# Optimization experiments

Hardware: AMD Instinct MI355X
Metric: run time of the kernel (lower is better)

## Reference

```python
import jax, jax.numpy as jnp
import numpy as np

N, TX, TZ, DX, DZ, DATT, DOUT = 8, 2048, 2048, 1024, 1024, 1024, 1024


def setup_inputs() -> dict:
    key = jax.random.key(0)
    ks = jax.random.split(key, 8)
    s = 0.02
    x = jax.random.normal(ks[0], (N, TX, DX), dtype=jnp.float32)
    z = jax.random.normal(ks[1], (N, TZ, DZ), dtype=jnp.float32)
    Wq = jax.random.normal(ks[2], (DX, DATT), dtype=jnp.float32) * s
    bq = jnp.zeros((DATT,), dtype=jnp.float32)
    Wk = jax.random.normal(ks[3], (DZ, DATT), dtype=jnp.float32) * s
    bk = jnp.zeros((DATT,), dtype=jnp.float32)
    Wv = jax.random.normal(ks[4], (DZ, DOUT), dtype=jnp.float32) * s
    bv = jnp.zeros((DOUT,), dtype=jnp.float32)
    # fixed boolean mask [Tx, Tz]; causal lower-triangular so no row is fully masked
    mask = jnp.tril(jnp.ones((TX, TZ), dtype=bool))
    return {"x": x, "z": z, "Wq": Wq, "bq": bq, "Wk": Wk, "bk": bk,
            "Wv": Wv, "bv": bv, "mask": mask}


def reference(x, z, Wq, bq, Wk, bk, Wv, bv, mask):
    Datt = Wq.shape[1]
    Q = x @ Wq + bq                      # [N, Tx, Datt]
    K = z @ Wk + bk                      # [N, Tz, Datt]
    V = z @ Wv + bv                      # [N, Tz, Dout]
    S = jnp.einsum('bxd,bzd->bxz', Q, K)  # [N, Tx, Tz]
    S = jnp.where(mask[None, :, :], S, -jnp.inf)
    A = jax.nn.softmax(S / jnp.sqrt(jnp.float32(Datt)), axis=-1)
    y = jnp.einsum('bxz,bzo->bxo', A, V)  # [N, Tx, Dout]
    return y
```

## Files before the change

### kernel.cpp

```cpp
#include <hip/hip_runtime.h>

typedef _Float16 f16;
typedef _Float16 f16x8 __attribute__((ext_vector_type(8)));
typedef _Float16 f16x4 __attribute__((ext_vector_type(4)));
typedef float    f32x4 __attribute__((ext_vector_type(4)));

constexpr int NB   = 8;
constexpr int T    = 2048;
constexpr int D    = 1024;
constexpr int NTRI = 136;

__device__ __forceinline__ void load_lds16(const f16* g, f16* l) {
    __builtin_amdgcn_global_load_lds(
        (const __attribute__((address_space(1))) void*)g,
        (__attribute__((address_space(3))) void*)l, 16, 0, 0);
}

__global__ __launch_bounds__(256) void cast_transpose_w(
    const float* __restrict__ W0, const float* __restrict__ W1,
    const float* __restrict__ W2, f16* __restrict__ Wt)
{
    __shared__ f16 tile[32][33];
    const int which = blockIdx.z;
    const float* W = which == 0 ? W0 : (which == 1 ? W1 : W2);
    f16* dst = Wt + (size_t)which * D * D;
    const int c0 = blockIdx.x * 32, r0 = blockIdx.y * 32;
    const int tx = threadIdx.x & 31, ty = threadIdx.x >> 5;
    #pragma unroll
    for (int i = 0; i < 32; i += 8)
        tile[ty + i][tx] = (f16)W[(size_t)(r0 + ty + i) * D + c0 + tx];
    __syncthreads();
    #pragma unroll
    for (int i = 0; i < 32; i += 8)
        dst[(size_t)(c0 + ty + i) * D + r0 + tx] = tile[tx][ty + i];
}

__global__ __launch_bounds__(256) void cast_xz(
    const float* __restrict__ x, const float* __restrict__ z,
    f16* __restrict__ xh, f16* __restrict__ zh)
{
    const float* src = blockIdx.y ? z : x;
    f16* dst = blockIdx.y ? zh : xh;
    const size_t i = ((size_t)blockIdx.x * 256 + threadIdx.x) * 4;
    const float4 v = *(const float4*)(src + i);
    f16x4 u = { (f16)v.x, (f16)v.y, (f16)v.z, (f16)v.w };
    *(f16x4*)(dst + i) = u;
}

template<int MODE>
__global__ __launch_bounds__(256) void gemm_nt(
    const f16* __restrict__ Ag_, const f16* __restrict__ Bg_,
    void* __restrict__ Cg_, void* __restrict__ Cg2_,
    const float* __restrict__ bias, const float* __restrict__ bias2,
    float* __restrict__ rsum)
{
    __shared__ f16 As[2 * 128 * 32];
    __shared__ f16 Bs[2 * 128 * 32];

    int bx, by;
    const int bz = blockIdx.z;
    if (MODE == 1) {
        const int idx = blockIdx.x;
        by = (int)((sqrtf(8.0f * idx + 1.0f) - 1.0f) * 0.5f);
        while ((by + 1) * (by + 2) / 2 <= idx) ++by;
        while (by * (by + 1) / 2 > idx) --by;
        bx = idx - by * (by + 1) / 2;
    } else if (MODE == 2) {
        bx = blockIdx.x; by = 15 - blockIdx.y;
    } else {
        constexpr int GX  = (MODE == 0) ? 8 : 16;
        constexpr int LGX = (MODE == 0) ? 3 : 4;
        constexpr int NWG = GX * 128;
        int id = (int)blockIdx.y * GX + (int)blockIdx.x;
        id = (id & 7) * (NWG >> 3) + (id >> 3);
        bx = id & (GX - 1);
        by = id >> LGX;
    }

    const size_t bm0 = (size_t)by * 128, bn0 = (size_t)bx * 128;
    const f16* Abase; const f16* Bbase;
    int lda, ldb, K;
    if (MODE == 0 || MODE == 4) {
        Abase = Ag_ + bm0 * D;                       lda = D;
        Bbase = Bg_ + bn0 * D;                       ldb = D; K = D;
    } else if (MODE == 1) {
        Abase = Ag_ + (size_t)bz * T * D + bm0 * D;  lda = D;
        Bbase = Bg_ + (size_t)bz * T * D + bn0 * D;  ldb = D; K = D;
    } else {
        Abase = Ag_ + ((size_t)bz * NTRI + (size_t)by * (by + 1) / 2) * 16384;
        lda = 128;
        Bbase = Bg_ + (size_t)bz * D * T + bn0 * T;  ldb = T;
        K = (by + 1) * 128;
    }

    const int t    = threadIdx.x;
    const int lane = t & 63, wave = t >> 6;
    const int wr   = (wave >> 1) * 64, wc = (wave & 1) * 64;
    const int fr   = lane & 15, fo = (lane >> 4) * 8;
    const int srow = t >> 2;
    const int scol = ((t & 3) ^ ((t >> 2) & 3)) * 8;
    const int wub  = (t & 192) * 8;
    const int fsw  = fo ^ ((fr & 3) << 3);
    const int arow = (wr + fr) * 32 + fsw;
    const int brow = (wc + fr) * 32 + fsw;

    f32x4 acc[4][4] = {};
    const int nk = K >> 5;

    auto stage = [&](int s, int b) {
        const int k = s * 32;
        const f16* Ak;
        if (MODE == 2) Ak = Abase + (size_t)(k >> 7) * 16384 + (k & 127);
        else           Ak = Abase + k;
        #pragma unroll
        for (int it = 0; it < 2; ++it)
            load_lds16(Ak + (size_t)(it * 64 + srow) * lda + scol,
                       As + b * 4096 + it * 2048 + wub);
        #pragma unroll
        for (int it = 0; it < 2; ++it)
            load_lds16(Bbase + k + (size_t)(it * 64 + srow) * ldb + scol,
                       Bs + b * 4096 + it * 2048 + wub);
    };

    stage(0, 0);
    __syncthreads();

    for (int s = 0; s < nk; ++s) {
        const int cur = s & 1;
        if (s + 1 < nk) stage(s + 1, cur ^ 1);

        f16x8 av[4], bv[4];
        #pragma unroll
        for (int i = 0; i < 4; ++i)
            av[i] = *(const f16x8*)&As[cur * 4096 + arow + i * 512];
        #pragma unroll
        for (int j = 0; j < 4; ++j)
            bv[j] = *(const f16x8*)&Bs[cur * 4096 + brow + j * 512];
        #pragma unroll
        for (int i = 0; i < 4; ++i)
            #pragma unroll
            for (int j = 0; j < 4; ++j)
                acc[i][j] = __builtin_amdgcn_mfma_f32_16x16x32_f16(av[i], bv[j], acc[i][j], 0, 0, 0);

        __syncthreads();
    }

    const int cr = (lane >> 4) * 4, cc = lane & 15;
    if (MODE == 0) {
        f16* Cp = (f16*)Cg_;
        #pragma unroll
        for (int j = 0; j < 4; ++j) {
            const int col = (int)bn0 + wc + j * 16 + cc;
            const float bb = bias[col];
            #pragma unroll
            for (int i = 0; i < 4; ++i)
                #pragma unroll
                for (int g = 0; g < 4; ++g)
                    Cp[(bm0 + wr + i * 16 + cr + g) * D + col] = (f16)(acc[i][j][g] + bb);
        }
    } else if (MODE == 4) {
        if (bx < 8) {
            f16* Cp = (f16*)Cg_;
            #pragma unroll
            for (int j = 0; j < 4; ++j) {
                const int col = (int)bn0 + wc + j * 16 + cc;
                const float bb = bias[col];
                #pragma unroll
                for (int i = 0; i < 4; ++i)
                    #pragma unroll
                    for (int g = 0; g < 4; ++g)
                        Cp[(bm0 + wr + i * 16 + cr + g) * D + col] = (f16)(acc[i][j][g] + bb);
            }
        } else {
            f16* Vt = (f16*)Cg2_;
            const int b  = (int)(bm0 >> 11);
            const int r0 = (int)(bm0 & 2047);
            #pragma unroll
            for (int j = 0; j < 4; ++j) {
                const int colv = (int)bn0 - 1024 + wc + j * 16 + cc;
                const float bb = bias2[colv];
                #pragma unroll
                for (int i = 0; i < 4; ++i) {
                    f16x4 pk = { (f16)(acc[i][j][0] + bb), (f16)(acc[i][j][1] + bb),
                                 (f16)(acc[i][j][2] + bb), (f16)(acc[i][j][3] + bb) };
                    *(f16x4*)&Vt[(size_t)b * D * T + (size_t)colv * T + r0 + wr + i * 16 + cr] = pk;
                }
            }
        }
    } else if (MODE == 1) {
        f16* Cp = (f16*)Cg_ + ((size_t)bz * NTRI + (size_t)by * (by + 1) / 2 + bx) * 16384;
        float* rs = rsum + (size_t)bz * T + bm0;
        float rowsum[4][4] = {};
        #pragma unroll
        for (int i = 0; i < 4; ++i)
            #pragma unroll
            for (int j = 0; j < 4; ++j)
                #pragma unroll
                for (int g = 0; g < 4; ++g) {
                    const int lr = wr + i * 16 + cr + g, lc = wc + j * 16 + cc;
                    const int r = (int)bm0 + lr, c = (int)bn0 + lc;
                    const float p = (c > r) ? 0.0f : __expf(acc[i][j][g] * 0.03125f);
                    Cp[lr * 128 + lc] = (f16)p;
                    rowsum[i][g] += p;
                }
        #pragma unroll
        for (int i = 0; i < 4; ++i)
            #pragma unroll
            for (int g = 0; g < 4; ++g) {
                float s = rowsum[i][g];
                s += __shfl_xor(s, 1, 64);
                s += __shfl_xor(s, 2, 64);
                s += __shfl_xor(s, 4, 64);
                s += __shfl_xor(s, 8, 64);
                if (cc == 0) atomicAdd(&rs[wr + i * 16 + cr + g], s);
            }
    } else {
        float* Cp = (float*)Cg_ + (size_t)bz * T * D;
        const float* rs = rsum + (size_t)bz * T;
        #pragma unroll
        for (int i = 0; i < 4; ++i) {
            const int r4 = (int)bm0 + wr + i * 16 + cr;
            float rinv[4];
            #pragma unroll
            for (int g = 0; g < 4; ++g) rinv[g] = 1.0f / rs[r4 + g];
            #pragma unroll
            for (int j = 0; j < 4; ++j)
                #pragma unroll
                for (int g = 0; g < 4; ++g)
                    Cp[(size_t)(r4 + g) * D + bn0 + wc + j * 16 + cc] = acc[i][j][g] * rinv[g];
        }
    }
}

extern "C" void kernel_launch(void* const* d_in, const int* in_sizes, int n_in,
                              void* d_out, int out_size, void* d_ws, size_t ws_size,
                              hipStream_t stream)
{
    const float* x  = (const float*)d_in[0];
    const float* z  = (const float*)d_in[1];
    const float* Wq = (const float*)d_in[2];
    const float* bq = (const float*)d_in[3];
    const float* Wk = (const float*)d_in[4];
    const float* bk = (const float*)d_in[5];
    const float* Wv = (const float*)d_in[6];
    const float* bv = (const float*)d_in[7];
    float* out = (float*)d_out;

    char* ws = (char*)d_ws;
    f16*   Wt   = (f16*)(ws);
    f16*   xh   = (f16*)(ws + 6291456ull);
    f16*   zh   = (f16*)(ws + 39845888ull);
    f16*   Qh   = (f16*)(ws + 73400320ull);
    f16*   Kh   = (f16*)(ws + 106954752ull);
    f16*   Vt   = (f16*)(ws + 140509184ull);
    f16*   SA   = (f16*)(ws + 174063616ull);
    float* rsum = (float*)(ws + 209715200ull);

    hipMemsetAsync(rsum, 0, (size_t)NB * T * sizeof(float), stream);
    cast_transpose_w<<<dim3(32, 32, 3), 256, 0, stream>>>(Wq, Wk, Wv, Wt);
    cast_xz<<<dim3(16384, 2, 1), 256, 0, stream>>>(x, z, xh, zh);
    gemm_nt<0><<<dim3(8, 128, 1), 256, 0, stream>>>(xh, Wt, Qh, nullptr, bq, nullptr, nullptr);
    gemm_nt<4><<<dim3(16, 128, 1), 256, 0, stream>>>(zh, Wt + 1048576, Kh, Vt, bk, bv, nullptr);
    gemm_nt<1><<<dim3(136, 1, 8), 256, 0, stream>>>(Qh, Kh, SA, nullptr, nullptr, nullptr, rsum);
    gemm_nt<2><<<dim3(8, 16, 8), 256, 0, stream>>>(SA, Vt, out, nullptr, nullptr, nullptr, rsum);
}
```

Baseline: 553.1 us.

## Enlarge GEMM tiles to 256x256x64 with 512 threads and finer barrier sync

All four GEMM stages move from 128x128x32 tiles with 4 waves to 256x256x64 tiles with 8 waves, each wave computing a 128x64 sub-tile. The aim is higher data reuse per LDS load and fewer global loads per FLOP. The probability matrix SA becomes a row-panel layout with a variable leading dimension, placed in workspace that is reused from the earlier cast buffers. The loop now waits on vmcnt with raw s_barrier and raises wave priority around the MFMA blocks. The trade-offs are 128KB of LDS per block, fewer blocks per stage, and coarser load balance on the triangular stages.

```diff
diff --git a/kernel.cpp b/kernel.cpp
--- a/kernel.cpp
+++ b/kernel.cpp
@@ -8,7 +8,7 @@
 constexpr int NB   = 8;
 constexpr int T    = 2048;
 constexpr int D    = 1024;
-constexpr int NTRI = 136;
+constexpr int SA_BATCH = 36 * 65536;
 
 __device__ __forceinline__ void load_lds16(const f16* g, f16* l) {
     __builtin_amdgcn_global_load_lds(
@@ -48,14 +48,14 @@
 }
 
 template<int MODE>
-__global__ __launch_bounds__(256) void gemm_nt(
+__global__ __launch_bounds__(512, 2) void gemm_nt(
     const f16* __restrict__ Ag_, const f16* __restrict__ Bg_,
     void* __restrict__ Cg_, void* __restrict__ Cg2_,
     const float* __restrict__ bias, const float* __restrict__ bias2,
     float* __restrict__ rsum)
 {
-    __shared__ f16 As[2 * 128 * 32];
-    __shared__ f16 Bs[2 * 128 * 32];
+    __shared__ f16 As[2 * 256 * 64];
+    __shared__ f16 Bs[2 * 256 * 64];
 
     int bx, by;
     const int bz = blockIdx.z;
@@ -66,18 +66,18 @@
         while (by * (by + 1) / 2 > idx) --by;
         bx = idx - by * (by + 1) / 2;
     } else if (MODE == 2) {
-        bx = blockIdx.x; by = 15 - blockIdx.y;
+        bx = blockIdx.x; by = 7 - blockIdx.y;
     } else {
-        constexpr int GX  = (MODE == 0) ? 8 : 16;
-        constexpr int LGX = (MODE == 0) ? 3 : 4;
-        constexpr int NWG = GX * 128;
+        constexpr int GX  = (MODE == 0) ? 4 : 8;
+        constexpr int LGX = (MODE == 0) ? 2 : 3;
+        constexpr int NWG = GX * 64;
         int id = (int)blockIdx.y * GX + (int)blockIdx.x;
         id = (id & 7) * (NWG >> 3) + (id >> 3);
         bx = id & (GX - 1);
         by = id >> LGX;
     }
 
-    const size_t bm0 = (size_t)by * 128, bn0 = (size_t)bx * 128;
+    const size_t bm0 = (size_t)by * 256, bn0 = (size_t)bx * 256;
     const f16* Abase; const f16* Bbase;
     int lda, ldb, K;
     if (MODE == 0 || MODE == 4) {
@@ -87,62 +87,73 @@
         Abase = Ag_ + (size_t)bz * T * D + bm0 * D;  lda = D;
         Bbase = Bg_ + (size_t)bz * T * D + bn0 * D;  ldb = D; K = D;
     } else {
-        Abase = Ag_ + ((size_t)bz * NTRI + (size_t)by * (by + 1) / 2) * 16384;
-        lda = 128;
+        K = (by + 1) * 256; lda = K;
+        Abase = Ag_ + (size_t)bz * SA_BATCH + (size_t)(by * (by + 1) / 2) * 65536;
         Bbase = Bg_ + (size_t)bz * D * T + bn0 * T;  ldb = T;
-        K = (by + 1) * 128;
     }
 
     const int t    = threadIdx.x;
     const int lane = t & 63, wave = t >> 6;
-    const int wr   = (wave >> 1) * 64, wc = (wave & 1) * 64;
-    const int fr   = lane & 15, fo = (lane >> 4) * 8;
-    const int srow = t >> 2;
-    const int scol = ((t & 3) ^ ((t >> 2) & 3)) * 8;
-    const int wub  = (t & 192) * 8;
-    const int fsw  = fo ^ ((fr & 3) << 3);
-    const int arow = (wr + fr) * 32 + fsw;
-    const int brow = (wc + fr) * 32 + fsw;
-
-    f32x4 acc[4][4] = {};
-    const int nk = K >> 5;
+    const int wr   = (wave >> 2) * 128, wc = (wave & 3) * 64;
+    const int fr   = lane & 15, ho = lane >> 4;
+    const int srow = t >> 3;
+    const int scol = ((t & 7) ^ ((t >> 3) & 7)) * 8;
+    const int wub  = wave * 512;
+    const f16* Ap = Abase + (size_t)srow * lda + scol;
+    const f16* Bp = Bbase + (size_t)srow * ldb + scol;
+    const int fsw = fr & 7;
+
+    f32x4 acc[8][4] = {};
+    const int nk = K >> 6;
 
     auto stage = [&](int s, int b) {
-        const int k = s * 32;
-        const f16* Ak;
-        if (MODE == 2) Ak = Abase + (size_t)(k >> 7) * 16384 + (k & 127);
-        else           Ak = Abase + k;
-        #pragma unroll
-        for (int it = 0; it < 2; ++it)
-            load_lds16(Ak + (size_t)(it * 64 + srow) * lda + scol,
-                       As + b * 4096 + it * 2048 + wub);
-        #pragma unroll
-        for (int it = 0; it < 2; ++it)
-            load_lds16(Bbase + k + (size_t)(it * 64 + srow) * ldb + scol,
-                       Bs + b * 4096 + it * 2048 + wub);
+        const size_t k = (size_t)s * 64;
+        #pragma unroll
+        for (int i = 0; i < 4; ++i)
+            load_lds16(Ap + k + (size_t)(i * 64) * lda,
+                       As + b * 16384 + i * 4096 + wub);
+        #pragma unroll
+        for (int i = 0; i < 4; ++i)
+            load_lds16(Bp + k + (size_t)(i * 64) * ldb,
+                       Bs + b * 16384 + i * 4096 + wub);
     };
 
     stage(0, 0);
-    __syncthreads();
 
     for (int s = 0; s < nk; ++s) {
         const int cur = s & 1;
-        if (s + 1 < nk) stage(s + 1, cur ^ 1);
-
-        f16x8 av[4], bv[4];
-        #pragma unroll
-        for (int i = 0; i < 4; ++i)
-            av[i] = *(const f16x8*)&As[cur * 4096 + arow + i * 512];
-        #pragma unroll
-        for (int j = 0; j < 4; ++j)
-            bv[j] = *(const f16x8*)&Bs[cur * 4096 + brow + j * 512];
-        #pragma unroll
-        for (int i = 0; i < 4; ++i)
+        if (s + 1 < nk) {
+            stage(s + 1, cur ^ 1);
+            asm volatile("s_waitcnt vmcnt(8)" ::: "memory");
+        } else {
+            asm volatile("s_waitcnt vmcnt(0)" ::: "memory");
+        }
+        __builtin_amdgcn_sched_barrier(0);
+        __builtin_amdgcn_s_barrier();
+        __builtin_amdgcn_sched_barrier(0);
+
+        const f16* Ab = As + cur * 16384;
+        const f16* Bb = Bs + cur * 16384;
+        #pragma unroll
+        for (int kc = 0; kc < 2; ++kc) {
+            const int ch = (((kc << 2) | ho) ^ fsw) << 3;
+            f16x8 av[8], bv[4];
+            #pragma unroll
+            for (int i = 0; i < 8; ++i)
+                av[i] = *(const f16x8*)&Ab[((wr + i * 16 + fr) << 6) + ch];
             #pragma unroll
             for (int j = 0; j < 4; ++j)
-                acc[i][j] = __builtin_amdgcn_mfma_f32_16x16x32_f16(av[i], bv[j], acc[i][j], 0, 0, 0);
-
-        __syncthreads();
+                bv[j] = *(const f16x8*)&Bb[((wc + j * 16 + fr) << 6) + ch];
+            __builtin_amdgcn_s_setprio(1);
+            #pragma unroll
+            for (int i = 0; i < 8; ++i)
+                #pragma unroll
+                for (int j = 0; j < 4; ++j)
+                    acc[i][j] = __builtin_amdgcn_mfma_f32_16x16x32_f16(av[i], bv[j], acc[i][j], 0, 0, 0);
+            __builtin_amdgcn_s_setprio(0);
+        }
+        __builtin_amdgcn_sched_barrier(0);
+        __builtin_amdgcn_s_barrier();
     }
 
     const int cr = (lane >> 4) * 4, cc = lane & 15;
@@ -153,20 +164,20 @@
             const int col = (int)bn0 + wc + j * 16 + cc;
             const float bb = bias[col];
             #pragma unroll
-            for (int i = 0; i < 4; ++i)
+            for (int i = 0; i < 8; ++i)
                 #pragma unroll
                 for (int g = 0; g < 4; ++g)
                     Cp[(bm0 + wr + i * 16 + cr + g) * D + col] = (f16)(acc[i][j][g] + bb);
         }
     } else if (MODE == 4) {
-        if (bx < 8) {
+        if (bx < 4) {
             f16* Cp = (f16*)Cg_;
             #pragma unroll
             for (int j = 0; j < 4; ++j) {
                 const int col = (int)bn0 + wc + j * 16 + cc;
                 const float bb = bias[col];
                 #pragma unroll
-                for (int i = 0; i < 4; ++i)
+                for (int i = 0; i < 8; ++i)
                     #pragma unroll
                     for (int g = 0; g < 4; ++g)
                         Cp[(bm0 + wr + i * 16 + cr + g) * D + col] = (f16)(acc[i][j][g] + bb);
@@ -180,7 +191,7 @@
                 const int colv = (int)bn0 - 1024 + wc + j * 16 + cc;
                 const float bb = bias2[colv];
                 #pragma unroll
-                for (int i = 0; i < 4; ++i) {
+                for (int i = 0; i < 8; ++i) {
                     f16x4 pk = { (f16)(acc[i][j][0] + bb), (f16)(acc[i][j][1] + bb),
                                  (f16)(acc[i][j][2] + bb), (f16)(acc[i][j][3] + bb) };
                     *(f16x4*)&Vt[(size_t)b * D * T + (size_t)colv * T + r0 + wr + i * 16 + cr] = pk;
@@ -188,11 +199,13 @@
             }
         }
     } else if (MODE == 1) {
-        f16* Cp = (f16*)Cg_ + ((size_t)bz * NTRI + (size_t)by * (by + 1) / 2 + bx) * 16384;
+        const int ldab = (by + 1) * 256;
+        f16* Cp = (f16*)Cg_ + (size_t)bz * SA_BATCH
+                + (size_t)(by * (by + 1) / 2) * 65536 + bn0;
         float* rs = rsum + (size_t)bz * T + bm0;
-        float rowsum[4][4] = {};
-        #pragma unroll
-        for (int i = 0; i < 4; ++i)
+        #pragma unroll
+        for (int i = 0; i < 8; ++i) {
+            float rowsum[4] = {};
             #pragma unroll
             for (int j = 0; j < 4; ++j)
                 #pragma unroll
@@ -200,25 +213,24 @@
                     const int lr = wr + i * 16 + cr + g, lc = wc + j * 16 + cc;
                     const int r = (int)bm0 + lr, c = (int)bn0 + lc;
                     const float p = (c > r) ? 0.0f : __expf(acc[i][j][g] * 0.03125f);
-                    Cp[lr * 128 + lc] = (f16)p;
-                    rowsum[i][g] += p;
+                    Cp[(size_t)lr * ldab + lc] = (f16)p;
+                    rowsum[g] += p;
                 }
-        #pragma unroll
-        for (int i = 0; i < 4; ++i)
             #pragma unroll
             for (int g = 0; g < 4; ++g) {
-                float s = rowsum[i][g];
-                s += __shfl_xor(s, 1, 64);
-                s += __shfl_xor(s, 2, 64);
-                s += __shfl_xor(s, 4, 64);
-                s += __shfl_xor(s, 8, 64);
-                if (cc == 0) atomicAdd(&rs[wr + i * 16 + cr + g], s);
+                float sv = rowsum[g];
+                sv += __shfl_xor(sv, 1, 64);
+                sv += __shfl_xor(sv, 2, 64);
+                sv += __shfl_xor(sv, 4, 64);
+                sv += __shfl_xor(sv, 8, 64);
+                if (cc == 0) atomicAdd(&rs[wr + i * 16 + cr + g], sv);
             }
+        }
     } else {
         float* Cp = (float*)Cg_ + (size_t)bz * T * D;
         const float* rs = rsum + (size_t)bz * T;
         #pragma unroll
-        for (int i = 0; i < 4; ++i) {
+        for (int i = 0; i < 8; ++i) {
             const int r4 = (int)bm0 + wr + i * 16 + cr;
             float rinv[4];
             #pragma unroll
@@ -253,14 +265,14 @@
     f16*   Qh   = (f16*)(ws + 73400320ull);
     f16*   Kh   = (f16*)(ws + 106954752ull);
     f16*   Vt   = (f16*)(ws + 140509184ull);
-    f16*   SA   = (f16*)(ws + 174063616ull);
+    f16*   SA   = (f16*)(ws + 6291456ull);
     float* rsum = (float*)(ws + 209715200ull);
 
     hipMemsetAsync(rsum, 0, (size_t)NB * T * sizeof(float), stream);
     cast_transpose_w<<<dim3(32, 32, 3), 256, 0, stream>>>(Wq, Wk, Wv, Wt);
     cast_xz<<<dim3(16384, 2, 1), 256, 0, stream>>>(x, z, xh, zh);
-    gemm_nt<0><<<dim3(8, 128, 1), 256, 0, stream>>>(xh, Wt, Qh, nullptr, bq, nullptr, nullptr);
-    gemm_nt<4><<<dim3(16, 128, 1), 256, 0, stream>>>(zh, Wt + 1048576, Kh, Vt, bk, bv, nullptr);
-    gemm_nt<1><<<dim3(136, 1, 8), 256, 0, stream>>>(Qh, Kh, SA, nullptr, nullptr, nullptr, rsum);
-    gemm_nt<2><<<dim3(8, 16, 8), 256, 0, stream>>>(SA, Vt, out, nullptr, nullptr, nullptr, rsum);
-}
+    gemm_nt<0><<<dim3(4, 64, 1), 512, 0, stream>>>(xh, Wt, Qh, nullptr, bq, nullptr, nullptr);
+    gemm_nt<4><<<dim3(8, 64, 1), 512, 0, stream>>>(zh, Wt + 1048576, Kh, Vt, bk, bv, nullptr);
+    gemm_nt<1><<<dim3(36, 1, 8), 512, 0, stream>>>(Qh, Kh, SA, nullptr, nullptr, nullptr, rsum);
+    gemm_nt<2><<<dim3(4, 8, 8), 512, 0, stream>>>(SA, Vt, out, nullptr, nullptr, nullptr, rsum);
+}
```

Result: faster. 463.5 us (-16.2%).
